# Performance work log

Measured on AMD Instinct MI355X. Metric: run time of the kernel, lower is better.

The kernel has to match this reference:

```python
import jax, jax.numpy as jnp
import numpy as np

B, S, C, D = 16, 8192, 32, 3
VEC_OUT = 16
OUT_CH = 128
NEG_SLOPE = 0.2
EPS = float(np.finfo(np.float64).eps)


def setup_inputs() -> dict:
    key = jax.random.key(0)
    k1, k2, k3, k4, k5 = jax.random.split(key, 5)
    x = jax.random.normal(k1, (B, S, C, D), dtype=jnp.float32)
    x = x / jnp.linalg.norm(x, axis=-1, keepdims=True)  # project onto S^2
    n_in = C - 1  # 31
    U0 = (jax.random.truncated_normal(k2, -2.0, 2.0, (VEC_OUT, n_in)) * np.sqrt(2.0 / n_in)).astype(jnp.float32)
    W0 = (jax.random.truncated_normal(k3, -2.0, 2.0, (VEC_OUT, n_in)) / np.sqrt(n_in) + 1.0 / n_in).astype(jnp.float32)
    feat = n_in * VEC_OUT  # 496
    dense_kernel = (jax.random.normal(k4, (feat, OUT_CH)) / np.sqrt(feat)).astype(jnp.float32)
    dense_bias = jnp.zeros((OUT_CH,), dtype=jnp.float32)
    return {"x": x, "U0": U0, "W0": W0, "dense_kernel": dense_kernel, "dense_bias": dense_bias}


def _sphere_log(p, q):
    # p: [N, D] base points, q: [N, C-1, D]; log_p(q) on unit sphere
    cos = jnp.clip(jnp.sum(p[:, None, :] * q, axis=-1), -1.0, 1.0)  # [N, C-1]
    theta = jnp.arccos(cos)
    sin_safe = jnp.where(theta < 1e-6, 1.0, jnp.sin(theta))
    fac = jnp.where(theta < 1e-6, 1.0, theta / sin_safe)
    return fac[..., None] * (q - cos[..., None] * p[:, None, :])  # [N, C-1, D]


def _vn_layer(w, U, W):
    # w: [B, S, n_in, D]
    k = jnp.einsum('ij,bsjd->bsid', U, w)
    q = jnp.einsum('ij,bsjd->bsid', W, w)
    sqnrm_k = jnp.sum(k * k, axis=-1, keepdims=True) + EPS
    dot_qk = jnp.sum(q * k, axis=-1, keepdims=True)
    h = q + k * jax.nn.relu(-dot_qk) / sqnrm_k
    return NEG_SLOPE * q + (1.0 - NEG_SLOPE) * h


def reference(x, U0, W0, dense_kernel, dense_bias):
    n_batch, n_seq, n_in = x.shape[:3]
    xf = x.reshape(-1, n_in, D)            # [N, C, D]
    p = xf[:, 0]                           # base points
    v = _sphere_log(p, xf[:, 1:])          # [N, C-1, D]
    w = v.reshape(n_batch, n_seq, n_in - 1, D)
    w = _vn_layer(w, U0, W0)               # [B, S, VEC_OUT, D]
    w = w.reshape(n_batch * n_seq, VEC_OUT, D)
    # metric.flat on the sphere (induced metric) is the identity; VEC_OUT <= n_in so flat applies to w
    y = jnp.einsum('nij,nkj->nik', v, w)   # [N, C-1, VEC_OUT]
    y = y.reshape(n_batch, n_seq, -1)
    return y @ dense_kernel + dense_bias   # [B, S, OUT_CH]
```

## Files before the change

### kernel.cpp

```cpp
#include <hip/hip_runtime.h>

typedef float float4v __attribute__((ext_vector_type(4)));
typedef short short8  __attribute__((ext_vector_type(8)));

#define NBLOCKS 512
#define TOK_PER_BLOCK 256
#define WS_NEEDED 131072

__device__ __forceinline__ short f2bf(float f) {
  unsigned u = __float_as_uint(f);
  return (short)((u + 0x7fffu + ((u >> 16) & 1u)) >> 16);
}

__global__ void dk_prep(const float* __restrict__ dk, short8* __restrict__ ws) {
  int g = blockIdx.x * 256 + threadIdx.x;
  int c = g & 127, k8g = (g >> 7) & 3, kk = g >> 9;
  short8 t;
#pragma unroll
  for (int j = 0; j < 8; ++j) {
    int f = kk * 32 + k8g * 8 + j;
    t[j] = (f < 496) ? f2bf(dk[f * 128 + c]) : (short)0;
  }
  ws[g] = t;
}

template<bool USE_WS>
__global__ __launch_bounds__(512, 4)
void tangent_fused(const float* __restrict__ x,
                   const float* __restrict__ U0,
                   const float* __restrict__ W0,
                   const float* __restrict__ dk,
                   const short8* __restrict__ wsdk,
                   const float* __restrict__ bias,
                   float* __restrict__ out)
{
  __shared__ __align__(16) float xlds[32 * 100];
  __shared__ __align__(16) float vlds[32 * 104];
  __shared__ __align__(16) float u0p[16 * 36];
  __shared__ __align__(16) float w0p[16 * 36];
  __shared__ __align__(16) short ylds[32 * 520];

  const int tid  = threadIdx.x;
  const int lane = tid & 63;
  const int wv   = tid >> 6;

  if (tid < 576) { u0p[tid] = 0.f; w0p[tid] = 0.f; }
  __syncthreads();
  if (tid < 496) {
    int r = tid / 31, c = tid % 31;
    u0p[r * 36 + c] = U0[tid];
    w0p[r * 36 + c] = W0[tid];
  }

  const int bn  = lane & 15;
  const int k8g = lane >> 4;
  const int k8  = k8g * 8;
  const int ch0 = wv * 16;
  short8 bfrag[16];
  if (USE_WS) {
#pragma unroll
    for (int kk = 0; kk < 16; ++kk)
      bfrag[kk] = wsdk[(kk * 4 + k8g) * 128 + ch0 + bn];
  } else {
#pragma unroll
    for (int kk = 0; kk < 16; ++kk) {
      short8 t;
#pragma unroll
      for (int j = 0; j < 8; ++j) {
        int f = kk * 32 + k8 + j;
        t[j] = (f < 496) ? f2bf(dk[f * 128 + ch0 + bn]) : (short)0;
      }
      bfrag[kk] = t;
    }
  }
  const float bias0 = bias[ch0 + bn];
  __syncthreads();

  const int trow = tid >> 4;
  const int tt   = tid & 15;
  const int block_tok0 = blockIdx.x * TOK_PER_BLOCK;

  for (int tile = 0; tile < 8; ++tile) {
    const int tbase = block_tok0 + tile * 32;

    {
      const float4v* xg = (const float4v*)(x + (size_t)tbase * 96);
      {
        int idx = tid;
        float4v v = xg[idx];
        *(float4v*)&xlds[(idx / 24) * 100 + (idx % 24) * 4] = v;
      }
      {
        int idx = tid + 512;
        if (idx < 768) {
          float4v v = xg[idx];
          *(float4v*)&xlds[(idx / 24) * 100 + (idx % 24) * 4] = v;
        }
      }
    }
    __syncthreads();

    {
      const float* xr = &xlds[trow * 100];
      float p0 = xr[0], p1 = xr[1], p2 = xr[2];
      float* vr = &vlds[trow * 104];
#pragma unroll
      for (int rep = 0; rep < 2; ++rep) {
        int jj = tt + rep * 16;
        if (jj < 31) {
          float q0 = xr[3 + 3 * jj], q1 = xr[4 + 3 * jj], q2 = xr[5 + 3 * jj];
          float cs = __fadd_rn(__fadd_rn(__fmul_rn(p0, q0), __fmul_rn(p1, q1)),
                               __fmul_rn(p2, q2));
          cs = fminf(fmaxf(cs, -1.f), 1.f);
          float th = acosf(cs);
          float fac = (th < 1e-6f) ? 1.f
                                   : th * rsqrtf((1.f - cs) * (1.f + cs));
          vr[3 * jj + 0] = fac * (q0 - cs * p0);
          vr[3 * jj + 1] = fac * (q1 - cs * p1);
          vr[3 * jj + 2] = fac * (q2 - cs * p2);
        }
      }
      if (tt == 15) { vr[93] = 0.f; vr[94] = 0.f; vr[95] = 0.f; }
    }

    {
      const float4v* v4 = (const float4v*)&vlds[trow * 104];
      const float4v* u4 = (const float4v*)&u0p[tt * 36];
      const float4v* w4 = (const float4v*)&w0p[tt * 36];
      float k0 = 0, k1 = 0, k2 = 0, q0 = 0, q1 = 0, q2 = 0;
#pragma unroll
      for (int g = 0; g < 8; ++g) {
        float4v a = v4[3 * g], b = v4[3 * g + 1], c = v4[3 * g + 2];
        float4v uu = u4[g], ww = w4[g];
        k0 += uu.x * a.x; k1 += uu.x * a.y; k2 += uu.x * a.z;
        q0 += ww.x * a.x; q1 += ww.x * a.y; q2 += ww.x * a.z;
        k0 += uu.y * a.w; k1 += uu.y * b.x; k2 += uu.y * b.y;
        q0 += ww.y * a.w; q1 += ww.y * b.x; q2 += ww.y * b.y;
        k0 += uu.z * b.z; k1 += uu.z * b.w; k2 += uu.z * c.x;
        q0 += ww.z * b.z; q1 += ww.z * b.w; q2 += ww.z * c.x;
        k0 += uu.w * c.y; k1 += uu.w * c.z; k2 += uu.w * c.w;
        q0 += ww.w * c.y; q1 += ww.w * c.z; q2 += ww.w * c.w;
      }
      float dot = k0 * q0 + k1 * q1 + k2 * q2;
      float sq  = k0 * k0 + k1 * k1 + k2 * k2 + 2.2204460492503131e-16f;
      float f8  = 0.8f * (fmaxf(-dot, 0.f) / sq);
      float wx = q0 + f8 * k0, wy = q1 + f8 * k1, wz = q2 + f8 * k2;

      asm volatile("" ::: "memory");

      short* yrow = &ylds[trow * 520];
#pragma unroll
      for (int g = 0; g < 8; ++g) {
        float4v a = v4[3 * g], b = v4[3 * g + 1], c = v4[3 * g + 2];
        float y0 = a.x * wx + a.y * wy + a.z * wz;
        float y1 = a.w * wx + b.x * wy + b.y * wz;
        float y2 = b.z * wx + b.w * wy + c.x * wz;
        float y3 = c.y * wx + c.z * wy + c.w * wz;
        yrow[(4 * g + 0) * 16 + tt] = f2bf(y0);
        yrow[(4 * g + 1) * 16 + tt] = f2bf(y1);
        yrow[(4 * g + 2) * 16 + tt] = f2bf(y2);
        yrow[(4 * g + 3) * 16 + tt] = f2bf(y3);
      }
    }
    __syncthreads();

    {
      const int am = lane & 15;
      float4v acc0 = {0.f, 0.f, 0.f, 0.f};
      float4v acc1 = {0.f, 0.f, 0.f, 0.f};
#pragma unroll
      for (int kk = 0; kk < 16; ++kk) {
        short8 a0 = *(const short8*)&ylds[am * 520 + kk * 32 + k8];
        short8 a1 = *(const short8*)&ylds[(16 + am) * 520 + kk * 32 + k8];
        acc0 = __builtin_amdgcn_mfma_f32_16x16x32_bf16(a0, bfrag[kk], acc0, 0, 0, 0);
        acc1 = __builtin_amdgcn_mfma_f32_16x16x32_bf16(a1, bfrag[kk], acc1, 0, 0, 0);
      }
      const int row4 = k8g * 4;
#pragma unroll
      for (int r = 0; r < 4; ++r) {
        out[(size_t)(tbase + row4 + r) * 128 + ch0 + bn]      = acc0[r] + bias0;
        out[(size_t)(tbase + 16 + row4 + r) * 128 + ch0 + bn] = acc1[r] + bias0;
      }
    }
  }
}

extern "C" void kernel_launch(void* const* d_in, const int* in_sizes, int n_in,
                              void* d_out, int out_size, void* d_ws, size_t ws_size,
                              hipStream_t stream) {
  const float* x    = (const float*)d_in[0];
  const float* U0   = (const float*)d_in[1];
  const float* W0   = (const float*)d_in[2];
  const float* dk   = (const float*)d_in[3];
  const float* bias = (const float*)d_in[4];
  float* out = (float*)d_out;
  if (ws_size >= WS_NEEDED) {
    short8* ws = (short8*)d_ws;
    dk_prep<<<32, 256, 0, stream>>>(dk, ws);
    tangent_fused<true><<<NBLOCKS, 512, 0, stream>>>(x, U0, W0, dk, ws, bias, out);
  } else {
    tangent_fused<false><<<NBLOCKS, 512, 0, stream>>>(x, U0, W0, dk, nullptr, bias, out);
  }
}
```

Baseline: 150.6 us.

## Prefetch next x tile into registers and compute tangent vectors in place

The next 32-token tile of x is loaded into registers while the current tile is processed, so global load latency overlaps with compute instead of stalling at the top of each iteration. The separate vlds buffer is removed and the sphere-log results are written back into xlds, which cuts shared-memory use per block. The launch bound rises from 4 to 6 waves so more blocks can be resident. The cost is higher register pressure, with a risk of spills given the 16 preloaded B fragments, and an in-place overwrite that depends on each row's 16 lanes reading before writing within one wavefront.

```diff
diff --git a/kernel.cpp b/kernel.cpp
--- a/kernel.cpp
+++ b/kernel.cpp
@@ -25,7 +25,7 @@
 }
 
 template<bool USE_WS>
-__global__ __launch_bounds__(512, 4)
+__global__ __launch_bounds__(512, 6)
 void tangent_fused(const float* __restrict__ x,
                    const float* __restrict__ U0,
                    const float* __restrict__ W0,
@@ -35,7 +35,6 @@
                    float* __restrict__ out)
 {
   __shared__ __align__(16) float xlds[32 * 100];
-  __shared__ __align__(16) float vlds[32 * 104];
   __shared__ __align__(16) float u0p[16 * 36];
   __shared__ __align__(16) float w0p[16 * 36];
   __shared__ __align__(16) short ylds[32 * 520];
@@ -44,7 +43,7 @@
   const int lane = tid & 63;
   const int wv   = tid >> 6;
 
-  if (tid < 576) { u0p[tid] = 0.f; w0p[tid] = 0.f; }
+  for (int i = tid; i < 576; i += 512) { u0p[i] = 0.f; w0p[i] = 0.f; }
   __syncthreads();
   if (tid < 496) {
     int r = tid / 31, c = tid % 31;
@@ -80,51 +79,63 @@
   const int tt   = tid & 15;
   const int block_tok0 = blockIdx.x * TOK_PER_BLOCK;
 
+  float4v pf0, pf1;
+  {
+    const float4v* xg = (const float4v*)(x + (size_t)block_tok0 * 96);
+    pf0 = xg[tid];
+    if (tid < 256) pf1 = xg[tid + 512];
+  }
+
   for (int tile = 0; tile < 8; ++tile) {
     const int tbase = block_tok0 + tile * 32;
 
+    *(float4v*)&xlds[(tid / 24) * 100 + (tid % 24) * 4] = pf0;
+    if (tid < 256) {
+      int idx = tid + 512;
+      *(float4v*)&xlds[(idx / 24) * 100 + (idx % 24) * 4] = pf1;
+    }
+    __syncthreads();
+
+    if (tile + 1 < 8) {
+      const float4v* xg = (const float4v*)(x + (size_t)(tbase + 32) * 96);
+      pf0 = xg[tid];
+      if (tid < 256) pf1 = xg[tid + 512];
+    }
+
     {
-      const float4v* xg = (const float4v*)(x + (size_t)tbase * 96);
-      {
-        int idx = tid;
-        float4v v = xg[idx];
-        *(float4v*)&xlds[(idx / 24) * 100 + (idx % 24) * 4] = v;
-      }
-      {
-        int idx = tid + 512;
-        if (idx < 768) {
-          float4v v = xg[idx];
-          *(float4v*)&xlds[(idx / 24) * 100 + (idx % 24) * 4] = v;
-        }
-      }
-    }
-    __syncthreads();
+      float* xr = &xlds[trow * 100];
+      float p0 = xr[0], p1 = xr[1], p2 = xr[2];
+      const int j0 = tt;
+      const int j1 = tt + 16;
+      float a0 = xr[3 + 3 * j0], a1 = xr[4 + 3 * j0], a2 = xr[5 + 3 * j0];
+      float b0 = xr[3 + 3 * j1], b1 = xr[4 + 3 * j1], b2 = xr[5 + 3 * j1];
+      asm volatile("" ::: "memory");
+
+      float cs0 = __fadd_rn(__fadd_rn(__fmul_rn(p0, a0), __fmul_rn(p1, a1)),
+                            __fmul_rn(p2, a2));
+      cs0 = fminf(fmaxf(cs0, -1.f), 1.f);
+      float th0 = acosf(cs0);
+      float fc0 = (th0 < 1e-6f) ? 1.f : th0 * rsqrtf((1.f - cs0) * (1.f + cs0));
+      xr[3 * j0 + 0] = fc0 * (a0 - cs0 * p0);
+      xr[3 * j0 + 1] = fc0 * (a1 - cs0 * p1);
+      xr[3 * j0 + 2] = fc0 * (a2 - cs0 * p2);
+
+      if (tt < 15) {
+        float cs1 = __fadd_rn(__fadd_rn(__fmul_rn(p0, b0), __fmul_rn(p1, b1)),
+                              __fmul_rn(p2, b2));
+        cs1 = fminf(fmaxf(cs1, -1.f), 1.f);
+        float th1 = acosf(cs1);
+        float fc1 = (th1 < 1e-6f) ? 1.f : th1 * rsqrtf((1.f - cs1) * (1.f + cs1));
+        xr[3 * j1 + 0] = fc1 * (b0 - cs1 * p0);
+        xr[3 * j1 + 1] = fc1 * (b1 - cs1 * p1);
+        xr[3 * j1 + 2] = fc1 * (b2 - cs1 * p2);
+      } else {
+        xr[93] = 0.f; xr[94] = 0.f; xr[95] = 0.f;
+      }
+    }
 
     {
-      const float* xr = &xlds[trow * 100];
-      float p0 = xr[0], p1 = xr[1], p2 = xr[2];
-      float* vr = &vlds[trow * 104];
-#pragma unroll
-      for (int rep = 0; rep < 2; ++rep) {
-        int jj = tt + rep * 16;
-        if (jj < 31) {
-          float q0 = xr[3 + 3 * jj], q1 = xr[4 + 3 * jj], q2 = xr[5 + 3 * jj];
-          float cs = __fadd_rn(__fadd_rn(__fmul_rn(p0, q0), __fmul_rn(p1, q1)),
-                               __fmul_rn(p2, q2));
-          cs = fminf(fmaxf(cs, -1.f), 1.f);
-          float th = acosf(cs);
-          float fac = (th < 1e-6f) ? 1.f
-                                   : th * rsqrtf((1.f - cs) * (1.f + cs));
-          vr[3 * jj + 0] = fac * (q0 - cs * p0);
-          vr[3 * jj + 1] = fac * (q1 - cs * p1);
-          vr[3 * jj + 2] = fac * (q2 - cs * p2);
-        }
-      }
-      if (tt == 15) { vr[93] = 0.f; vr[94] = 0.f; vr[95] = 0.f; }
-    }
-
-    {
-      const float4v* v4 = (const float4v*)&vlds[trow * 104];
+      const float4v* v4 = (const float4v*)&xlds[trow * 100];
       const float4v* u4 = (const float4v*)&u0p[tt * 36];
       const float4v* w4 = (const float4v*)&w0p[tt * 36];
       float k0 = 0, k1 = 0, k2 = 0, q0 = 0, q1 = 0, q2 = 0;
```

Result: slower. 203.9 us (+35.4%).
